# Kernel optimization log

Hardware: AMD Instinct MI355X
Metric: run time of the kernel (lower is better)

The kernel has to match this reference:

```python
import jax, jax.numpy as jnp
import numpy as np

N_NODES = 100000
N_EDGES = 1200000
IN_CH, HID_CH, OUT_CH = 64, 64, 32


def setup_inputs() -> dict:
    key = jax.random.key(0)
    ks = jax.random.split(key, 8)
    x = jax.random.normal(ks[0], (N_NODES, IN_CH), dtype=jnp.float32)
    edge_index = jax.random.randint(ks[1], (2, N_EDGES), 0, N_NODES, dtype=jnp.int64)
    # SAGEConv params: lin_l acts on aggregated neighbors (has bias), lin_r on root features.
    def glorot(k, fan_in, fan_out):
        s = jnp.sqrt(6.0 / (fan_in + fan_out))
        return jax.random.uniform(k, (fan_in, fan_out), jnp.float32, -s, s)
    W1_l = glorot(ks[2], IN_CH, HID_CH)
    W1_r = glorot(ks[3], IN_CH, HID_CH)
    b1 = jnp.zeros((HID_CH,), jnp.float32)
    W2_l = glorot(ks[4], HID_CH, OUT_CH)
    W2_r = glorot(ks[5], HID_CH, OUT_CH)
    b2 = jnp.zeros((OUT_CH,), jnp.float32)
    return {"x": x, "edge_index": edge_index, "W1_l": W1_l, "W1_r": W1_r,
            "b1": b1, "W2_l": W2_l, "W2_r": W2_r, "b2": b2}


def _sage_conv(h, src, dst, W_l, W_r, b):
    # gather source-node features along edges, mean-aggregate at destinations
    msg = h[src]                                               # [E, d]
    agg = jax.ops.segment_sum(msg, dst, num_segments=N_NODES)  # [N, d]
    cnt = jax.ops.segment_sum(jnp.ones((msg.shape[0],), h.dtype), dst,
                              num_segments=N_NODES)
    agg = agg / jnp.maximum(cnt, 1.0)[:, None]                 # mean (0 if no neighbors)
    return agg @ W_l + h @ W_r + b


def reference(x, edge_index, W1_l, W1_r, b1, W2_l, W2_r, b2):
    src, dst = edge_index[0], edge_index[1]
    h = _sage_conv(x, src, dst, W1_l, W1_r, b1)
    h = jax.nn.relu(h)
    # dropout is identity in eval mode
    return _sage_conv(h, src, dst, W2_l, W2_r, b2)
```

## Files before the change

kernel.cpp:

```cpp
#include <hip/hip_runtime.h>

__device__ __forceinline__ float bf2f(unsigned short u) {
    union { unsigned int i; float f; } v;
    v.i = ((unsigned int)u) << 16;
    return v.f;
}
__device__ __forceinline__ unsigned short f2bf(float f) {
    union { float f; unsigned int u; } v;
    v.f = f;
    unsigned int u = v.u;
    u += 0x7FFFu + ((u >> 16) & 1u);
    return (unsigned short)(u >> 16);
}
__device__ __forceinline__ unsigned int pack2bf(float lo, float hi) {
    return (unsigned int)f2bf(lo) | ((unsigned int)f2bf(hi) << 16);
}
__device__ __forceinline__ float loadElem(const void* p, size_t i, int isb) {
    return isb ? bf2f(((const unsigned short*)p)[i]) : ((const float*)p)[i];
}
__device__ __forceinline__ float bflo(unsigned int u) {
    union { unsigned int i; float f; } v; v.i = u << 16; return v.f;
}
__device__ __forceinline__ float bfhi(unsigned int u) {
    union { unsigned int i; float f; } v; v.i = u & 0xFFFF0000u; return v.f;
}

typedef __attribute__((ext_vector_type(8))) short bf16x8;
typedef __attribute__((ext_vector_type(4))) float f32x4;

#define CHUNK 4096
#define BSHIFT 8

__global__ void k_detect(const int* __restrict__ ei, int newords,
                         const unsigned int* __restrict__ xw, int nxw,
                         int* __restrict__ flags) {
    __shared__ int aOr;
    __shared__ int plaus;
    if (threadIdx.x == 0) { aOr = 0; plaus = 0; }
    __syncthreads();
    int v = 0;
    for (int i = 1 + 2 * (int)threadIdx.x; i < newords; i += 512) v |= ei[i];
    int pl = 0;
    for (int i = threadIdx.x; i < nxw; i += 256) {
        unsigned short lo = (unsigned short)(xw[i] & 0xFFFFu);
        float a = fabsf(bf2f(lo));
        if (a > 1e-5f && a < 100.0f) pl++;
    }
    atomicOr(&aOr, v);
    atomicAdd(&plaus, pl);
    __syncthreads();
    if (threadIdx.x == 0) {
        flags[0] = (aOr == 0) ? 1 : 0;
        flags[1] = (2 * plaus >= nxw) ? 1 : 0;
    }
}

__global__ void k_cast(const void* __restrict__ x, unsigned short* __restrict__ xb,
                       int n8, const int* __restrict__ flags) {
    int i = blockIdx.x * blockDim.x + threadIdx.x;
    if (i >= n8) return;
    if (flags[1]) {
        ((uint4*)xb)[i] = ((const uint4*)x)[i];
    } else {
        const float4* xf = (const float4*)x;
        float4 a = xf[2 * i], b = xf[2 * i + 1];
        ushort4 lo = { f2bf(a.x), f2bf(a.y), f2bf(a.z), f2bf(a.w) };
        ushort4 hi = { f2bf(b.x), f2bf(b.y), f2bf(b.z), f2bf(b.w) };
        ((ushort4*)xb)[2 * i] = lo;
        ((ushort4*)xb)[2 * i + 1] = hi;
    }
}

__global__ __launch_bounds__(256) void k_bcount(
        const int* __restrict__ ei, const int* __restrict__ flags,
        int* __restrict__ blockHist, int E, int NBUK, int nblk) {
    __shared__ int hist[512];
    int t = threadIdx.x;
    for (int i = t; i < NBUK; i += 256) hist[i] = 0;
    __syncthreads();
    int q = flags[0];
    int e0 = blockIdx.x * CHUNK, e1 = min(E, e0 + CHUNK);
    for (int e = e0 + t; e < e1; e += 256) {
        int dst = ei[((size_t)(E + e)) << q];
        atomicAdd(&hist[dst >> BSHIFT], 1);
    }
    __syncthreads();
    for (int i = t; i < NBUK; i += 256)
        blockHist[(size_t)i * nblk + blockIdx.x] = hist[i];
}

__global__ __launch_bounds__(256) void k_rowscan(
        int* __restrict__ blockHist, int* __restrict__ bukTot, int nblk) {
    __shared__ int sh[256];
    int t = threadIdx.x;
    int* row = blockHist + (size_t)blockIdx.x * nblk;
    int carry = 0;
    for (int base = 0; base < nblk; base += 256) {
        int i = base + t;
        int v = (i < nblk) ? row[i] : 0;
        sh[t] = v;
        __syncthreads();
        for (int off = 1; off < 256; off <<= 1) {
            int u = (t >= off) ? sh[t - off] : 0;
            __syncthreads();
            sh[t] += u;
            __syncthreads();
        }
        if (i < nblk) row[i] = carry + sh[t] - v;
        int tot = sh[255];
        __syncthreads();
        carry += tot;
    }
    if (t == 0) bukTot[blockIdx.x] = carry;
}

__global__ __launch_bounds__(512) void k_toto(
        const int* __restrict__ bukTot, int* __restrict__ bukOff,
        int* __restrict__ rowptr, int NBUK, int E, int N,
        const void* __restrict__ W1l, const void* __restrict__ W1r,
        const void* __restrict__ b1,
        const void* __restrict__ W2l, const void* __restrict__ W2r,
        const void* __restrict__ b2,
        unsigned short* __restrict__ wt1l, unsigned short* __restrict__ wt1r,
        unsigned short* __restrict__ wt2lr,
        float* __restrict__ bs1, float* __restrict__ bs2,
        const int* __restrict__ flags) {
    __shared__ int sh[512];
    int t = threadIdx.x;
    int v = (t < NBUK) ? bukTot[t] : 0;
    sh[t] = v;
    __syncthreads();
    for (int off = 1; off < 512; off <<= 1) {
        int u = (t >= off) ? sh[t - off] : 0;
        __syncthreads();
        sh[t] += u;
        __syncthreads();
    }
    if (t < NBUK) bukOff[t] = sh[t] - v;
    if (t == 0) { bukOff[NBUK] = E; rowptr[N] = E; }

    int isb = flags[1];
    for (int i = t; i < 64 * 64; i += 512) {
        int c = i >> 6, k = i & 63;
        wt1l[c * 72 + k] = isb ? ((const unsigned short*)W1l)[k * 64 + c]
                               : f2bf(((const float*)W1l)[k * 64 + c]);
        wt1r[c * 72 + k] = isb ? ((const unsigned short*)W1r)[k * 64 + c]
                               : f2bf(((const float*)W1r)[k * 64 + c]);
    }
    for (int i = t; i < 32 * 64; i += 512) {
        int c = i >> 6, k = i & 63;
        wt2lr[c * 72 + k]        = isb ? ((const unsigned short*)W2l)[k * 32 + c]
                                       : f2bf(((const float*)W2l)[k * 32 + c]);
        wt2lr[(32 + c) * 72 + k] = isb ? ((const unsigned short*)W2r)[k * 32 + c]
                                       : f2bf(((const float*)W2r)[k * 32 + c]);
    }
    if (t < 64) bs1[t] = loadElem(b1, t, isb);
    if (t < 32) bs2[t] = loadElem(b2, t, isb);
}

__global__ __launch_bounds__(256) void k_part(
        const int* __restrict__ ei, const int* __restrict__ flags,
        const int* __restrict__ blockHist, const int* __restrict__ bukOff,
        unsigned int* __restrict__ recs, int E, int NBUK, int nblk) {
    __shared__ int cur[512];
    int t = threadIdx.x;
    for (int i = t; i < NBUK; i += 256)
        cur[i] = blockHist[(size_t)i * nblk + blockIdx.x] + bukOff[i];
    __syncthreads();
    int q = flags[0];
    int e0 = blockIdx.x * CHUNK, e1 = min(E, e0 + CHUNK);
    for (int e = e0 + t; e < e1; e += 256) {
        int dst = ei[((size_t)(E + e)) << q];
        int src = ei[((size_t)e) << q];
        int pos = atomicAdd(&cur[dst >> BSHIFT], 1);
        recs[pos] = ((unsigned int)src << BSHIFT) | (unsigned int)(dst & ((1 << BSHIFT) - 1));
    }
}

__global__ __launch_bounds__(256) void k_csr(
        const unsigned int* __restrict__ recs, const int* __restrict__ bukOff,
        int* __restrict__ rowptr, int* __restrict__ esorted, int N) {
    __shared__ int degLoc[256];
    __shared__ int offLoc[256];
    __shared__ int wcur[256];
    int t = threadIdx.x;
    int node0 = blockIdx.x << BSHIFT;
    int r0 = bukOff[blockIdx.x], r1 = bukOff[blockIdx.x + 1];
    degLoc[t] = 0;
    __syncthreads();
    for (int i = r0 + t; i < r1; i += 256)
        atomicAdd(&degLoc[recs[i] & 255], 1);
    __syncthreads();
    int v = degLoc[t];
    offLoc[t] = v;
    __syncthreads();
    for (int off = 1; off < 256; off <<= 1) {
        int u = (t >= off) ? offLoc[t - off] : 0;
        __syncthreads();
        offLoc[t] += u;
        __syncthreads();
    }
    int excl = offLoc[t] - v;
    int node = node0 + t;
    if (node < N) rowptr[node] = r0 + excl;
    wcur[t] = r0 + excl;
    __syncthreads();
    for (int i = r0 + t; i < r1; i += 256) {
        unsigned int rec = recs[i];
        int pos = atomicAdd(&wcur[rec & 255], 1);
        esorted[pos] = (int)(rec >> BSHIFT);
    }
}

__global__ __launch_bounds__(256) void k_fused1(
        const unsigned short* __restrict__ feat,
        const int* __restrict__ rowptr,
        const int* __restrict__ esorted,
        const unsigned short* __restrict__ wt1l,
        const unsigned short* __restrict__ wt1r,
        const unsigned short* __restrict__ wt2lr,
        const float* __restrict__ bs1,
        const float* __restrict__ bs2,
        unsigned short* __restrict__ zbuf,
        unsigned short* __restrict__ gbuf,
        int N) {
    constexpr int SA2 = 72;
    constexpr int SW  = 72;
    __shared__ __align__(16) unsigned short amB16[64 * SA2];
    __shared__ __align__(16) unsigned short wT[64 * SW];
    __shared__ float Bs[64];
    __shared__ float Bs2[32];

    int t = threadIdx.x;
    int node0 = blockIdx.x << 6;

    for (int i = t; i < 576; i += 256)
        ((uint4*)wT)[i] = ((const uint4*)wt1l)[i];
    if (t < 64) Bs[t] = bs1[t];
    if (t >= 64 && t < 96) Bs2[t - 64] = bs2[t - 64];

    {
        int g = t >> 3, l = t & 7;
        const unsigned short* fl = feat + 8 * l;
#pragma unroll
        for (int jj = 0; jj < 2; ++jj) {
            int nl = g + 32 * jj;
            int node = node0 + nl;
            float a0 = 0.f, a1 = 0.f, a2 = 0.f, a3 = 0.f;
            float a4 = 0.f, a5 = 0.f, a6 = 0.f, a7 = 0.f;
            float inv = 0.f;
            if (node < N) {
                int beg = rowptr[node], end = rowptr[node + 1];
                int d = end - beg;
                if (d > 0) {
                    inv = 1.0f / (float)d;
                    for (int bs = beg; bs < end; bs += 8) {
                        int cnt = min(end - bs, 8);
                        const int* ep = esorted + bs;
                        int dd = 0;
                        if (cnt == 8) {
                            int s0 = ep[0], s1 = ep[1], s2 = ep[2], s3 = ep[3];
                            int s4 = ep[4], s5 = ep[5], s6 = ep[6], s7 = ep[7];
                            uint4 u0 = *(const uint4*)(fl + (size_t)s0 * 64);
                            uint4 u1 = *(const uint4*)(fl + (size_t)s1 * 64);
                            uint4 u2 = *(const uint4*)(fl + (size_t)s2 * 64);
                            uint4 u3 = *(const uint4*)(fl + (size_t)s3 * 64);
                            uint4 u4 = *(const uint4*)(fl + (size_t)s4 * 64);
                            uint4 u5 = *(const uint4*)(fl + (size_t)s5 * 64);
                            uint4 u6 = *(const uint4*)(fl + (size_t)s6 * 64);
                            uint4 u7 = *(const uint4*)(fl + (size_t)s7 * 64);
                            a0 += bflo(u0.x) + bflo(u1.x) + bflo(u2.x) + bflo(u3.x)
                                + bflo(u4.x) + bflo(u5.x) + bflo(u6.x) + bflo(u7.x);
                            a1 += bfhi(u0.x) + bfhi(u1.x) + bfhi(u2.x) + bfhi(u3.x)
                                + bfhi(u4.x) + bfhi(u5.x) + bfhi(u6.x) + bfhi(u7.x);
                            a2 += bflo(u0.y) + bflo(u1.y) + bflo(u2.y) + bflo(u3.y)
                                + bflo(u4.y) + bflo(u5.y) + bflo(u6.y) + bflo(u7.y);
                            a3 += bfhi(u0.y) + bfhi(u1.y) + bfhi(u2.y) + bfhi(u3.y)
                                + bfhi(u4.y) + bfhi(u5.y) + bfhi(u6.y) + bfhi(u7.y);
                            a4 += bflo(u0.z) + bflo(u1.z) + bflo(u2.z) + bflo(u3.z)
                                + bflo(u4.z) + bflo(u5.z) + bflo(u6.z) + bflo(u7.z);
                            a5 += bfhi(u0.z) + bfhi(u1.z) + bfhi(u2.z) + bfhi(u3.z)
                                + bfhi(u4.z) + bfhi(u5.z) + bfhi(u6.z) + bfhi(u7.z);
                            a6 += bflo(u0.w) + bflo(u1.w) + bflo(u2.w) + bflo(u3.w)
                                + bflo(u4.w) + bflo(u5.w) + bflo(u6.w) + bflo(u7.w);
                            a7 += bfhi(u0.w) + bfhi(u1.w) + bfhi(u2.w) + bfhi(u3.w)
                                + bfhi(u4.w) + bfhi(u5.w) + bfhi(u6.w) + bfhi(u7.w);
                            dd = 8;
                        }
                        for (; dd + 4 <= cnt; dd += 4) {
                            int s0 = ep[dd + 0], s1 = ep[dd + 1];
                            int s2 = ep[dd + 2], s3 = ep[dd + 3];
                            uint4 u0 = *(const uint4*)(fl + (size_t)s0 * 64);
                            uint4 u1 = *(const uint4*)(fl + (size_t)s1 * 64);
                            uint4 u2 = *(const uint4*)(fl + (size_t)s2 * 64);
                            uint4 u3 = *(const uint4*)(fl + (size_t)s3 * 64);
                            a0 += bflo(u0.x) + bflo(u1.x) + bflo(u2.x) + bflo(u3.x);
                            a1 += bfhi(u0.x) + bfhi(u1.x) + bfhi(u2.x) + bfhi(u3.x);
                            a2 += bflo(u0.y) + bflo(u1.y) + bflo(u2.y) + bflo(u3.y);
                            a3 += bfhi(u0.y) + bfhi(u1.y) + bfhi(u2.y) + bfhi(u3.y);
                            a4 += bflo(u0.z) + bflo(u1.z) + bflo(u2.z) + bflo(u3.z);
                            a5 += bfhi(u0.z) + bfhi(u1.z) + bfhi(u2.z) + bfhi(u3.z);
                            a6 += bflo(u0.w) + bflo(u1.w) + bflo(u2.w) + bflo(u3.w);
                            a7 += bfhi(u0.w) + bfhi(u1.w) + bfhi(u2.w) + bfhi(u3.w);
                        }
                        for (; dd < cnt; ++dd) {
                            int s = ep[dd];
                            uint4 u = *(const uint4*)(fl + (size_t)s * 64);
                            a0 += bflo(u.x); a1 += bfhi(u.x);
                            a2 += bflo(u.y); a3 += bfhi(u.y);
                            a4 += bflo(u.z); a5 += bfhi(u.z);
                            a6 += bflo(u.w); a7 += bfhi(u.w);
                        }
                    }
                }
            }
            uint4 packed = make_uint4(pack2bf(a0 * inv, a1 * inv),
                                      pack2bf(a2 * inv, a3 * inv),
                                      pack2bf(a4 * inv, a5 * inv),
                                      pack2bf(a6 * inv, a7 * inv));
            *(uint4*)&amB16[nl * SA2 + 8 * l] = packed;
        }
    }
    __syncthreads();

    int wid = t >> 6, lane = t & 63;
    int arow = lane & 15;
    int kgrp = (lane >> 4) * 8;
    f32x4 acc[4];
#pragma unroll
    for (int ct = 0; ct < 4; ++ct) acc[ct] = (f32x4){0.f, 0.f, 0.f, 0.f};

    const unsigned short* aBase = &amB16[(16 * wid + arow) * SA2 + kgrp];
#pragma unroll
    for (int kh = 0; kh < 2; ++kh) {
        bf16x8 a = *(const bf16x8*)(aBase + kh * 32);
#pragma unroll
        for (int ct = 0; ct < 4; ++ct) {
            bf16x8 b = *(const bf16x8*)&wT[(16 * ct + arow) * SW + kh * 32 + kgrp];
            acc[ct] = __builtin_amdgcn_mfma_f32_16x16x32_bf16(a, b, acc[ct], 0, 0, 0);
        }
    }
    __syncthreads();

    for (int i = t; i < 64 * 8; i += 256) {
        int nl = i >> 3, c = i & 7;
        int gn = node0 + nl;
        uint4 u = make_uint4(0u, 0u, 0u, 0u);
        if (gn < N) u = *(const uint4*)(feat + (size_t)gn * 64 + 8 * c);
        *(uint4*)&amB16[nl * SA2 + 8 * c] = u;
    }
    for (int i = t; i < 576; i += 256)
        ((uint4*)wT)[i] = ((const uint4*)wt1r)[i];
    __syncthreads();

#pragma unroll
    for (int kh = 0; kh < 2; ++kh) {
        bf16x8 a = *(const bf16x8*)(aBase + kh * 32);
#pragma unroll
        for (int ct = 0; ct < 4; ++ct) {
            bf16x8 b = *(const bf16x8*)&wT[(16 * ct + arow) * SW + kh * 32 + kgrp];
            acc[ct] = __builtin_amdgcn_mfma_f32_16x16x32_bf16(a, b, acc[ct], 0, 0, 0);
        }
    }
    __syncthreads();

    {
        int rbase = (lane >> 4) * 4;
#pragma unroll
        for (int ct = 0; ct < 4; ++ct) {
            int ch = 16 * ct + arow;
            float bv = Bs[ch];
#pragma unroll
            for (int r = 0; r < 4; ++r) {
                int nl = 16 * wid + rbase + r;
                float v = fmaxf(acc[ct][r] + bv, 0.f);
                amB16[nl * SA2 + ch] = f2bf(v);
            }
        }
    }
    for (int i = t; i < 576; i += 256)
        ((uint4*)wT)[i] = ((const uint4*)wt2lr)[i];
    __syncthreads();

    f32x4 accz[2], accg[2];
#pragma unroll
    for (int ct = 0; ct < 2; ++ct) {
        accz[ct] = (f32x4){0.f, 0.f, 0.f, 0.f};
        accg[ct] = (f32x4){0.f, 0.f, 0.f, 0.f};
    }
#pragma unroll
    for (int kh = 0; kh < 2; ++kh) {
        bf16x8 a = *(const bf16x8*)(aBase + kh * 32);
#pragma unroll
        for (int ct = 0; ct < 2; ++ct) {
            bf16x8 bz = *(const bf16x8*)&wT[(16 * ct + arow) * SW + kh * 32 + kgrp];
            bf16x8 bg = *(const bf16x8*)&wT[(32 + 16 * ct + arow) * SW + kh * 32 + kgrp];
            accz[ct] = __builtin_amdgcn_mfma_f32_16x16x32_bf16(a, bz, accz[ct], 0, 0, 0);
            accg[ct] = __builtin_amdgcn_mfma_f32_16x16x32_bf16(a, bg, accg[ct], 0, 0, 0);
        }
    }

#pragma unroll
    for (int ct = 0; ct < 2; ++ct) {
        int ch = 16 * ct + arow;
        float b2v = Bs2[ch];
#pragma unroll
        for (int r = 0; r < 4; ++r) {
            int node = node0 + 16 * wid + (lane >> 4) * 4 + r;
            if (node >= N) continue;
            zbuf[(size_t)node * 32 + ch] = f2bf(accz[ct][r]);
            gbuf[(size_t)node * 32 + ch] = f2bf(accg[ct][r] + b2v);
        }
    }
}

__global__ __launch_bounds__(256) void k_final(
        const unsigned short* __restrict__ zbuf,
        const unsigned short* __restrict__ gbuf,
        const int* __restrict__ rowptr,
        const int* __restrict__ esorted,
        void* __restrict__ outp,
        int N, const int* __restrict__ flags) {
    int t = threadIdx.x;
    int isb = flags[1];
    int node0 = blockIdx.x << 6;

    int g = t >> 3, l = t & 7;
    const unsigned short* fl = zbuf + 4 * l;
#pragma unroll
    for (int jj = 0; jj < 2; ++jj) {
        int nl = g + 32 * jj;
        int node = node0 + nl;
        if (node >= N) continue;
        float a0 = 0.f, a1 = 0.f, a2 = 0.f, a3 = 0.f;
        float inv = 0.f;
        int beg = rowptr[node], end = rowptr[node + 1];
        int d = end - beg;
        if (d > 0) {
            inv = 1.0f / (float)d;
            for (int bs = beg; bs < end; bs += 8) {
                int cnt = min(end - bs, 8);
                const int* ep = esorted + bs;
                int dd = 0;
                if (cnt == 8) {
                    int s0 = ep[0], s1 = ep[1], s2 = ep[2], s3 = ep[3];
                    int s4 = ep[4], s5 = ep[5], s6 = ep[6], s7 = ep[7];
                    uint2 u0 = *(const uint2*)(fl + (size_t)s0 * 32);
                    uint2 u1 = *(const uint2*)(fl + (size_t)s1 * 32);
                    uint2 u2 = *(const uint2*)(fl + (size_t)s2 * 32);
                    uint2 u3 = *(const uint2*)(fl + (size_t)s3 * 32);
                    uint2 u4 = *(const uint2*)(fl + (size_t)s4 * 32);
                    uint2 u5 = *(const uint2*)(fl + (size_t)s5 * 32);
                    uint2 u6 = *(const uint2*)(fl + (size_t)s6 * 32);
                    uint2 u7 = *(const uint2*)(fl + (size_t)s7 * 32);
                    a0 += bflo(u0.x) + bflo(u1.x) + bflo(u2.x) + bflo(u3.x)
                        + bflo(u4.x) + bflo(u5.x) + bflo(u6.x) + bflo(u7.x);
                    a1 += bfhi(u0.x) + bfhi(u1.x) + bfhi(u2.x) + bfhi(u3.x)
                        + bfhi(u4.x) + bfhi(u5.x) + bfhi(u6.x) + bfhi(u7.x);
                    a2 += bflo(u0.y) + bflo(u1.y) + bflo(u2.y) + bflo(u3.y)
                        + bflo(u4.y) + bflo(u5.y) + bflo(u6.y) + bflo(u7.y);
                    a3 += bfhi(u0.y) + bfhi(u1.y) + bfhi(u2.y) + bfhi(u3.y)
                        + bfhi(u4.y) + bfhi(u5.y) + bfhi(u6.y) + bfhi(u7.y);
                    dd = 8;
                }
                for (; dd + 4 <= cnt; dd += 4) {
                    int s0 = ep[dd + 0], s1 = ep[dd + 1];
                    int s2 = ep[dd + 2], s3 = ep[dd + 3];
                    uint2 u0 = *(const uint2*)(fl + (size_t)s0 * 32);
                    uint2 u1 = *(const uint2*)(fl + (size_t)s1 * 32);
                    uint2 u2 = *(const uint2*)(fl + (size_t)s2 * 32);
                    uint2 u3 = *(const uint2*)(fl + (size_t)s3 * 32);
                    a0 += bflo(u0.x) + bflo(u1.x) + bflo(u2.x) + bflo(u3.x);
                    a1 += bfhi(u0.x) + bfhi(u1.x) + bfhi(u2.x) + bfhi(u3.x);
                    a2 += bflo(u0.y) + bflo(u1.y) + bflo(u2.y) + bflo(u3.y);
                    a3 += bfhi(u0.y) + bfhi(u1.y) + bfhi(u2.y) + bfhi(u3.y);
                }
                for (; dd < cnt; ++dd) {
                    int s = ep[dd];
                    uint2 u = *(const uint2*)(fl + (size_t)s * 32);
                    a0 += bflo(u.x); a1 += bfhi(u.x);
                    a2 += bflo(u.y); a3 += bfhi(u.y);
                }
            }
        }
        uint2 gv = *(const uint2*)(gbuf + (size_t)node * 32 + 4 * l);
        float r0 = a0 * inv + bflo(gv.x);
        float r1 = a1 * inv + bfhi(gv.x);
        float r2 = a2 * inv + bflo(gv.y);
        float r3 = a3 * inv + bfhi(gv.y);
        if (!isb) {
            *(float4*)((float*)outp + (size_t)node * 32 + 4 * l) =
                make_float4(r0, r1, r2, r3);
        } else {
            ushort4 o = { f2bf(r0), f2bf(r1), f2bf(r2), f2bf(r3) };
            *(ushort4*)((unsigned short*)outp + (size_t)node * 32 + 4 * l) = o;
        }
    }
}

extern "C" void kernel_launch(void* const* d_in, const int* in_sizes, int n_in,
                              void* d_out, int out_size, void* d_ws, size_t ws_size,
                              hipStream_t stream) {
    const void* x   = d_in[0];
    const int*  ei  = (const int*)d_in[1];
    const void* W1l = d_in[2];
    const void* W1r = d_in[3];
    const void* b1  = d_in[4];
    const void* W2l = d_in[5];
    const void* W2r = d_in[6];
    const void* b2  = d_in[7];

    const int N = in_sizes[0] / 64;
    const int E = in_sizes[1] / 2;
    const int NBUK = (N + (1 << BSHIFT) - 1) >> BSHIFT;
    const int nblk = (E + CHUNK - 1) / CHUNK;

    char* base = (char*)d_ws;
    size_t off = 0;
    auto alloc = [&](size_t bytes) { size_t o = off; off = (off + bytes + 255) & ~(size_t)255; return o; };
    int* flags   = (int*)(base + alloc(256));
    int* bukTot  = (int*)(base + alloc((size_t)NBUK * 4));
    int* bukOff  = (int*)(base + alloc((size_t)(NBUK + 1) * 4));
    int* rowptr  = (int*)(base + alloc((size_t)(N + 1) * 4));
    unsigned int* recs = (unsigned int*)(base + alloc((size_t)E * 4));
    int* esorted = (int*)(base + alloc((size_t)E * 4));
    unsigned short* xb = (unsigned short*)(base + alloc((size_t)N * 64 * 2));
    unsigned short* h  = (unsigned short*)(base + alloc((size_t)N * 64 * 2));
    unsigned short* wt1l  = (unsigned short*)(base + alloc(64 * 72 * 2));
    unsigned short* wt1r  = (unsigned short*)(base + alloc(64 * 72 * 2));
    unsigned short* wt2lr = (unsigned short*)(base + alloc(64 * 72 * 2));
    float* bs1 = (float*)(base + alloc(64 * 4));
    float* bs2 = (float*)(base + alloc(32 * 4));
    (void)ws_size;

    unsigned short* zbuf = h;
    unsigned short* gbuf = h + (size_t)N * 32;

    int* blockHist = (int*)xb;

    const int B = 256;
    int nd = 2 * E; if (nd > 2048) nd = 2048;

    k_detect<<<1, 256, 0, stream>>>(ei, nd, (const unsigned int*)x, 512, flags);
    k_bcount<<<nblk, B, 0, stream>>>(ei, flags, blockHist, E, NBUK, nblk);
    k_rowscan<<<NBUK, B, 0, stream>>>(blockHist, bukTot, nblk);
    k_toto<<<1, 512, 0, stream>>>(bukTot, bukOff, rowptr, NBUK, E, N,
                                  W1l, W1r, b1, W2l, W2r, b2,
                                  wt1l, wt1r, wt2lr, bs1, bs2, flags);
    k_part<<<nblk, B, 0, stream>>>(ei, flags, blockHist, bukOff, recs, E, NBUK, nblk);
    k_cast<<<(N * 8 + B - 1) / B, B, 0, stream>>>(x, xb, N * 8, flags);
    k_csr<<<NBUK, B, 0, stream>>>(recs, bukOff, rowptr, esorted, N);

    const int ntile = (N + 63) / 64;
    k_fused1<<<ntile, B, 0, stream>>>(xb, rowptr, esorted,
                                      wt1l, wt1r, wt2lr, bs1, bs2,
                                      zbuf, gbuf, N);
    k_final<<<ntile, B, 0, stream>>>(zbuf, gbuf, rowptr, esorted, d_out, N, flags);
}
```

Baseline: 213.6 us.

## Merge CSR-building preprocessing kernels into one cooperative megakernel with grid syncs

Replaces seven small preprocessing launches (detect, bucket count, row scan, offsets and weight transpose, partition, cast, CSR build) with a single cooperative kernel that separates phases with grid-wide syncs. The goal is to cut per-launch overhead and idle gaps between tiny kernels. The cast now overlaps the bucket-count phase, and blockHist gets its own buffer instead of aliasing xb. In exchange, the grid is capped at max(NBUK, nblk), about 391 blocks, so the cast runs at lower parallelism. Each grid sync also carries its own cost, and cooperative launch limits occupancy.

Result: slower. 624.5 us (+192.4%).

```diff
diff --git a/kernel.cpp b/kernel.cpp
--- a/kernel.cpp
+++ b/kernel.cpp
@@ -1,4 +1,7 @@
 #include <hip/hip_runtime.h>
+#include <hip/hip_cooperative_groups.h>
+
+namespace cg = cooperative_groups;
 
 __device__ __forceinline__ float bf2f(unsigned short u) {
     union { unsigned int i; float f; } v;
@@ -31,184 +34,188 @@
 #define CHUNK 4096
 #define BSHIFT 8
 
-__global__ void k_detect(const int* __restrict__ ei, int newords,
-                         const unsigned int* __restrict__ xw, int nxw,
-                         int* __restrict__ flags) {
-    __shared__ int aOr;
-    __shared__ int plaus;
-    if (threadIdx.x == 0) { aOr = 0; plaus = 0; }
-    __syncthreads();
-    int v = 0;
-    for (int i = 1 + 2 * (int)threadIdx.x; i < newords; i += 512) v |= ei[i];
-    int pl = 0;
-    for (int i = threadIdx.x; i < nxw; i += 256) {
-        unsigned short lo = (unsigned short)(xw[i] & 0xFFFFu);
-        float a = fabsf(bf2f(lo));
-        if (a > 1e-5f && a < 100.0f) pl++;
-    }
-    atomicOr(&aOr, v);
-    atomicAdd(&plaus, pl);
-    __syncthreads();
-    if (threadIdx.x == 0) {
-        flags[0] = (aOr == 0) ? 1 : 0;
-        flags[1] = (2 * plaus >= nxw) ? 1 : 0;
-    }
-}
-
-__global__ void k_cast(const void* __restrict__ x, unsigned short* __restrict__ xb,
-                       int n8, const int* __restrict__ flags) {
-    int i = blockIdx.x * blockDim.x + threadIdx.x;
-    if (i >= n8) return;
-    if (flags[1]) {
-        ((uint4*)xb)[i] = ((const uint4*)x)[i];
-    } else {
-        const float4* xf = (const float4*)x;
-        float4 a = xf[2 * i], b = xf[2 * i + 1];
-        ushort4 lo = { f2bf(a.x), f2bf(a.y), f2bf(a.z), f2bf(a.w) };
-        ushort4 hi = { f2bf(b.x), f2bf(b.y), f2bf(b.z), f2bf(b.w) };
-        ((ushort4*)xb)[2 * i] = lo;
-        ((ushort4*)xb)[2 * i + 1] = hi;
-    }
-}
-
-__global__ __launch_bounds__(256) void k_bcount(
-        const int* __restrict__ ei, const int* __restrict__ flags,
-        int* __restrict__ blockHist, int E, int NBUK, int nblk) {
-    __shared__ int hist[512];
+struct MegaArgs {
+    const int* ei; const unsigned int* xw; int nd; int nxw;
+    int* flags;
+    int* blockHist; int* bukTot; int* bukOff; int* rowptr;
+    unsigned int* recs; int* esorted;
+    const void* x; unsigned short* xb;
+    const void* W1l; const void* W1r; const void* b1;
+    const void* W2l; const void* W2r; const void* b2;
+    unsigned short* wt1l; unsigned short* wt1r; unsigned short* wt2lr;
+    float* bs1; float* bs2;
+    int E; int N; int NBUK; int nblk; int n8;
+};
+
+__global__ __launch_bounds__(256) void k_mega(MegaArgs a) {
+    cg::grid_group gg = cg::this_grid();
+    __shared__ int sh[768];
     int t = threadIdx.x;
-    for (int i = t; i < NBUK; i += 256) hist[i] = 0;
-    __syncthreads();
-    int q = flags[0];
-    int e0 = blockIdx.x * CHUNK, e1 = min(E, e0 + CHUNK);
-    for (int e = e0 + t; e < e1; e += 256) {
-        int dst = ei[((size_t)(E + e)) << q];
-        atomicAdd(&hist[dst >> BSHIFT], 1);
-    }
-    __syncthreads();
-    for (int i = t; i < NBUK; i += 256)
-        blockHist[(size_t)i * nblk + blockIdx.x] = hist[i];
-}
-
-__global__ __launch_bounds__(256) void k_rowscan(
-        int* __restrict__ blockHist, int* __restrict__ bukTot, int nblk) {
-    __shared__ int sh[256];
-    int t = threadIdx.x;
-    int* row = blockHist + (size_t)blockIdx.x * nblk;
-    int carry = 0;
-    for (int base = 0; base < nblk; base += 256) {
-        int i = base + t;
-        int v = (i < nblk) ? row[i] : 0;
-        sh[t] = v;
+    int b = blockIdx.x;
+
+    if (b == 0) {
+        int v = 0;
+        for (int i = 1 + 2 * t; i < a.nd; i += 512) v |= a.ei[i];
+        int pl = 0;
+        for (int i = t; i < a.nxw; i += 256) {
+            unsigned short lo = (unsigned short)(a.xw[i] & 0xFFFFu);
+            float f = fabsf(bf2f(lo));
+            if (f > 1e-5f && f < 100.0f) pl++;
+        }
+        sh[t] = v; sh[256 + t] = pl;
+        __syncthreads();
+        for (int off = 128; off > 0; off >>= 1) {
+            if (t < off) { sh[t] |= sh[t + off]; sh[256 + t] += sh[256 + t + off]; }
+            __syncthreads();
+        }
+        if (t == 0) {
+            a.flags[0] = (sh[0] == 0) ? 1 : 0;
+            a.flags[1] = (2 * sh[256] >= a.nxw) ? 1 : 0;
+        }
+    }
+    __threadfence();
+    gg.sync();
+
+    int q = a.flags[0], isb = a.flags[1];
+
+    if (b < a.nblk) {
+        for (int i = t; i < a.NBUK; i += 256) sh[i] = 0;
+        __syncthreads();
+        int e0 = b * CHUNK, e1 = min(a.E, e0 + CHUNK);
+        for (int e = e0 + t; e < e1; e += 256) {
+            int dst = a.ei[((size_t)(a.E + e)) << q];
+            atomicAdd(&sh[dst >> BSHIFT], 1);
+        }
+        __syncthreads();
+        for (int i = t; i < a.NBUK; i += 256)
+            a.blockHist[(size_t)i * a.nblk + b] = sh[i];
+    }
+    for (int i = b * 256 + t; i < a.n8; i += gridDim.x * 256) {
+        if (isb) {
+            ((uint4*)a.xb)[i] = ((const uint4*)a.x)[i];
+        } else {
+            const float4* xf = (const float4*)a.x;
+            float4 p = xf[2 * i], r = xf[2 * i + 1];
+            ushort4 lo = { f2bf(p.x), f2bf(p.y), f2bf(p.z), f2bf(p.w) };
+            ushort4 hi = { f2bf(r.x), f2bf(r.y), f2bf(r.z), f2bf(r.w) };
+            ((ushort4*)a.xb)[2 * i] = lo;
+            ((ushort4*)a.xb)[2 * i + 1] = hi;
+        }
+    }
+    __threadfence();
+    gg.sync();
+
+    if (b < a.NBUK) {
+        int* row = a.blockHist + (size_t)b * a.nblk;
+        int carry = 0;
+        for (int base = 0; base < a.nblk; base += 256) {
+            int i = base + t;
+            int v = (i < a.nblk) ? row[i] : 0;
+            sh[t] = v;
+            __syncthreads();
+            for (int off = 1; off < 256; off <<= 1) {
+                int u = (t >= off) ? sh[t - off] : 0;
+                __syncthreads();
+                sh[t] += u;
+                __syncthreads();
+            }
+            if (i < a.nblk) row[i] = carry + sh[t] - v;
+            int tot = sh[255];
+            __syncthreads();
+            carry += tot;
+        }
+        if (t == 0) a.bukTot[b] = carry;
+    }
+    __threadfence();
+    gg.sync();
+
+    if (b == 0) {
+        int carry = 0;
+        for (int base = 0; base < a.NBUK; base += 256) {
+            int i = base + t;
+            int v = (i < a.NBUK) ? a.bukTot[i] : 0;
+            sh[t] = v;
+            __syncthreads();
+            for (int off = 1; off < 256; off <<= 1) {
+                int u = (t >= off) ? sh[t - off] : 0;
+                __syncthreads();
+                sh[t] += u;
+                __syncthreads();
+            }
+            if (i < a.NBUK) a.bukOff[i] = carry + sh[t] - v;
+            int tot = sh[255];
+            __syncthreads();
+            carry += tot;
+        }
+        if (t == 0) { a.bukOff[a.NBUK] = a.E; a.rowptr[a.N] = a.E; }
+    } else if (b == 1) {
+        for (int i = t; i < 64 * 64; i += 256) {
+            int c = i >> 6, k = i & 63;
+            a.wt1l[c * 72 + k] = isb ? ((const unsigned short*)a.W1l)[k * 64 + c]
+                                     : f2bf(((const float*)a.W1l)[k * 64 + c]);
+            a.wt1r[c * 72 + k] = isb ? ((const unsigned short*)a.W1r)[k * 64 + c]
+                                     : f2bf(((const float*)a.W1r)[k * 64 + c]);
+        }
+    } else if (b == 2) {
+        for (int i = t; i < 32 * 64; i += 256) {
+            int c = i >> 6, k = i & 63;
+            a.wt2lr[c * 72 + k]        = isb ? ((const unsigned short*)a.W2l)[k * 32 + c]
+                                             : f2bf(((const float*)a.W2l)[k * 32 + c]);
+            a.wt2lr[(32 + c) * 72 + k] = isb ? ((const unsigned short*)a.W2r)[k * 32 + c]
+                                             : f2bf(((const float*)a.W2r)[k * 32 + c]);
+        }
+        if (t < 64) a.bs1[t] = loadElem(a.b1, t, isb);
+        if (t >= 64 && t < 96) a.bs2[t - 64] = loadElem(a.b2, t - 64, isb);
+    }
+    __threadfence();
+    gg.sync();
+
+    if (b < a.nblk) {
+        for (int i = t; i < a.NBUK; i += 256)
+            sh[i] = a.blockHist[(size_t)i * a.nblk + b] + a.bukOff[i];
+        __syncthreads();
+        int e0 = b * CHUNK, e1 = min(a.E, e0 + CHUNK);
+        for (int e = e0 + t; e < e1; e += 256) {
+            int dst = a.ei[((size_t)(a.E + e)) << q];
+            int src = a.ei[((size_t)e) << q];
+            int pos = atomicAdd(&sh[dst >> BSHIFT], 1);
+            a.recs[pos] = ((unsigned int)src << BSHIFT) |
+                          (unsigned int)(dst & ((1 << BSHIFT) - 1));
+        }
+    }
+    __threadfence();
+    gg.sync();
+
+    if (b < a.NBUK) {
+        int node0 = b << BSHIFT;
+        int r0 = a.bukOff[b], r1 = a.bukOff[b + 1];
+        int* degLoc = sh;
+        int* offLoc = sh + 256;
+        int* wcur   = sh + 512;
+        degLoc[t] = 0;
+        __syncthreads();
+        for (int i = r0 + t; i < r1; i += 256)
+            atomicAdd(&degLoc[a.recs[i] & 255], 1);
+        __syncthreads();
+        int v = degLoc[t];
+        offLoc[t] = v;
         __syncthreads();
         for (int off = 1; off < 256; off <<= 1) {
-            int u = (t >= off) ? sh[t - off] : 0;
-            __syncthreads();
-            sh[t] += u;
-            __syncthreads();
-        }
-        if (i < nblk) row[i] = carry + sh[t] - v;
-        int tot = sh[255];
-        __syncthreads();
-        carry += tot;
-    }
-    if (t == 0) bukTot[blockIdx.x] = carry;
-}
-
-__global__ __launch_bounds__(512) void k_toto(
-        const int* __restrict__ bukTot, int* __restrict__ bukOff,
-        int* __restrict__ rowptr, int NBUK, int E, int N,
-        const void* __restrict__ W1l, const void* __restrict__ W1r,
-        const void* __restrict__ b1,
-        const void* __restrict__ W2l, const void* __restrict__ W2r,
-        const void* __restrict__ b2,
-        unsigned short* __restrict__ wt1l, unsigned short* __restrict__ wt1r,
-        unsigned short* __restrict__ wt2lr,
-        float* __restrict__ bs1, float* __restrict__ bs2,
-        const int* __restrict__ flags) {
-    __shared__ int sh[512];
-    int t = threadIdx.x;
-    int v = (t < NBUK) ? bukTot[t] : 0;
-    sh[t] = v;
-    __syncthreads();
-    for (int off = 1; off < 512; off <<= 1) {
-        int u = (t >= off) ? sh[t - off] : 0;
-        __syncthreads();
-        sh[t] += u;
-        __syncthreads();
-    }
-    if (t < NBUK) bukOff[t] = sh[t] - v;
-    if (t == 0) { bukOff[NBUK] = E; rowptr[N] = E; }
-
-    int isb = flags[1];
-    for (int i = t; i < 64 * 64; i += 512) {
-        int c = i >> 6, k = i & 63;
-        wt1l[c * 72 + k] = isb ? ((const unsigned short*)W1l)[k * 64 + c]
-                               : f2bf(((const float*)W1l)[k * 64 + c]);
-        wt1r[c * 72 + k] = isb ? ((const unsigned short*)W1r)[k * 64 + c]
-                               : f2bf(((const float*)W1r)[k * 64 + c]);
-    }
-    for (int i = t; i < 32 * 64; i += 512) {
-        int c = i >> 6, k = i & 63;
-        wt2lr[c * 72 + k]        = isb ? ((const unsigned short*)W2l)[k * 32 + c]
-                                       : f2bf(((const float*)W2l)[k * 32 + c]);
-        wt2lr[(32 + c) * 72 + k] = isb ? ((const unsigned short*)W2r)[k * 32 + c]
-                                       : f2bf(((const float*)W2r)[k * 32 + c]);
-    }
-    if (t < 64) bs1[t] = loadElem(b1, t, isb);
-    if (t < 32) bs2[t] = loadElem(b2, t, isb);
-}
-
-__global__ __launch_bounds__(256) void k_part(
-        const int* __restrict__ ei, const int* __restrict__ flags,
-        const int* __restrict__ blockHist, const int* __restrict__ bukOff,
-        unsigned int* __restrict__ recs, int E, int NBUK, int nblk) {
-    __shared__ int cur[512];
-    int t = threadIdx.x;
-    for (int i = t; i < NBUK; i += 256)
-        cur[i] = blockHist[(size_t)i * nblk + blockIdx.x] + bukOff[i];
-    __syncthreads();
-    int q = flags[0];
-    int e0 = blockIdx.x * CHUNK, e1 = min(E, e0 + CHUNK);
-    for (int e = e0 + t; e < e1; e += 256) {
-        int dst = ei[((size_t)(E + e)) << q];
-        int src = ei[((size_t)e) << q];
-        int pos = atomicAdd(&cur[dst >> BSHIFT], 1);
-        recs[pos] = ((unsigned int)src << BSHIFT) | (unsigned int)(dst & ((1 << BSHIFT) - 1));
-    }
-}
-
-__global__ __launch_bounds__(256) void k_csr(
-        const unsigned int* __restrict__ recs, const int* __restrict__ bukOff,
-        int* __restrict__ rowptr, int* __restrict__ esorted, int N) {
-    __shared__ int degLoc[256];
-    __shared__ int offLoc[256];
-    __shared__ int wcur[256];
-    int t = threadIdx.x;
-    int node0 = blockIdx.x << BSHIFT;
-    int r0 = bukOff[blockIdx.x], r1 = bukOff[blockIdx.x + 1];
-    degLoc[t] = 0;
-    __syncthreads();
-    for (int i = r0 + t; i < r1; i += 256)
-        atomicAdd(&degLoc[recs[i] & 255], 1);
-    __syncthreads();
-    int v = degLoc[t];
-    offLoc[t] = v;
-    __syncthreads();
-    for (int off = 1; off < 256; off <<= 1) {
-        int u = (t >= off) ? offLoc[t - off] : 0;
-        __syncthreads();
-        offLoc[t] += u;
-        __syncthreads();
-    }
-    int excl = offLoc[t] - v;
-    int node = node0 + t;
-    if (node < N) rowptr[node] = r0 + excl;
-    wcur[t] = r0 + excl;
-    __syncthreads();
-    for (int i = r0 + t; i < r1; i += 256) {
-        unsigned int rec = recs[i];
-        int pos = atomicAdd(&wcur[rec & 255], 1);
-        esorted[pos] = (int)(rec >> BSHIFT);
+            int u = (t >= off) ? offLoc[t - off] : 0;
+            __syncthreads();
+            offLoc[t] += u;
+            __syncthreads();
+        }
+        int excl = offLoc[t] - v;
+        int node = node0 + t;
+        if (node < a.N) a.rowptr[node] = r0 + excl;
+        wcur[t] = r0 + excl;
+        __syncthreads();
+        for (int i = r0 + t; i < r1; i += 256) {
+            unsigned int rec = a.recs[i];
+            int pos = atomicAdd(&wcur[rec & 255], 1);
+            a.esorted[pos] = (int)(rec >> BSHIFT);
+        }
     }
 }
 
@@ -336,8 +343,8 @@
         bf16x8 a = *(const bf16x8*)(aBase + kh * 32);
 #pragma unroll
         for (int ct = 0; ct < 4; ++ct) {
-            bf16x8 b = *(const bf16x8*)&wT[(16 * ct + arow) * SW + kh * 32 + kgrp];
-            acc[ct] = __builtin_amdgcn_mfma_f32_16x16x32_bf16(a, b, acc[ct], 0, 0, 0);
+            bf16x8 bb = *(const bf16x8*)&wT[(16 * ct + arow) * SW + kh * 32 + kgrp];
+            acc[ct] = __builtin_amdgcn_mfma_f32_16x16x32_bf16(a, bb, acc[ct], 0, 0, 0);
         }
     }
     __syncthreads();
@@ -358,8 +365,8 @@
         bf16x8 a = *(const bf16x8*)(aBase + kh * 32);
 #pragma unroll
         for (int ct = 0; ct < 4; ++ct) {
-            bf16x8 b = *(const bf16x8*)&wT[(16 * ct + arow) * SW + kh * 32 + kgrp];
-            acc[ct] = __builtin_amdgcn_mfma_f32_16x16x32_bf16(a, b, acc[ct], 0, 0, 0);
+            bf16x8 bb = *(const bf16x8*)&wT[(16 * ct + arow) * SW + kh * 32 + kgrp];
+            acc[ct] = __builtin_amdgcn_mfma_f32_16x16x32_bf16(a, bb, acc[ct], 0, 0, 0);
         }
     }
     __syncthreads();
@@ -531,29 +538,34 @@
     unsigned short* wt2lr = (unsigned short*)(base + alloc(64 * 72 * 2));
     float* bs1 = (float*)(base + alloc(64 * 4));
     float* bs2 = (float*)(base + alloc(32 * 4));
+    int* blockHist = (int*)(base + alloc((size_t)NBUK * nblk * 4));
     (void)ws_size;
 
     unsigned short* zbuf = h;
     unsigned short* gbuf = h + (size_t)N * 32;
 
-    int* blockHist = (int*)xb;
-
-    const int B = 256;
     int nd = 2 * E; if (nd > 2048) nd = 2048;
 
-    k_detect<<<1, 256, 0, stream>>>(ei, nd, (const unsigned int*)x, 512, flags);
-    k_bcount<<<nblk, B, 0, stream>>>(ei, flags, blockHist, E, NBUK, nblk);
-    k_rowscan<<<NBUK, B, 0, stream>>>(blockHist, bukTot, nblk);
-    k_toto<<<1, 512, 0, stream>>>(bukTot, bukOff, rowptr, NBUK, E, N,
-                                  W1l, W1r, b1, W2l, W2r, b2,
-                                  wt1l, wt1r, wt2lr, bs1, bs2, flags);
-    k_part<<<nblk, B, 0, stream>>>(ei, flags, blockHist, bukOff, recs, E, NBUK, nblk);
-    k_cast<<<(N * 8 + B - 1) / B, B, 0, stream>>>(x, xb, N * 8, flags);
-    k_csr<<<NBUK, B, 0, stream>>>(recs, bukOff, rowptr, esorted, N);
+    MegaArgs ma;
+    ma.ei = ei; ma.xw = (const unsigned int*)x; ma.nd = nd; ma.nxw = 512;
+    ma.flags = flags;
+    ma.blockHist = blockHist; ma.bukTot = bukTot; ma.bukOff = bukOff; ma.rowptr = rowptr;
+    ma.recs = recs; ma.esorted = esorted;
+    ma.x = x; ma.xb = xb;
+    ma.W1l = W1l; ma.W1r = W1r; ma.b1 = b1;
+    ma.W2l = W2l; ma.W2r = W2r; ma.b2 = b2;
+    ma.wt1l = wt1l; ma.wt1r = wt1r; ma.wt2lr = wt2lr;
+    ma.bs1 = bs1; ma.bs2 = bs2;
+    ma.E = E; ma.N = N; ma.NBUK = NBUK; ma.nblk = nblk; ma.n8 = N * 8;
+
+    int gmax = (NBUK > nblk) ? NBUK : nblk;
+    void* params[1] = { &ma };
+    hipLaunchCooperativeKernel((void*)k_mega, dim3(gmax), dim3(256),
+                               params, 0, stream);
 
     const int ntile = (N + 63) / 64;
-    k_fused1<<<ntile, B, 0, stream>>>(xb, rowptr, esorted,
-                                      wt1l, wt1r, wt2lr, bs1, bs2,
-                                      zbuf, gbuf, N);
-    k_final<<<ntile, B, 0, stream>>>(zbuf, gbuf, rowptr, esorted, d_out, N, flags);
-}
+    k_fused1<<<ntile, 256, 0, stream>>>(xb, rowptr, esorted,
+                                        wt1l, wt1r, wt2lr, bs1, bs2,
+                                        zbuf, gbuf, N);
+    k_final<<<ntile, 256, 0, stream>>>(zbuf, gbuf, rowptr, esorted, d_out, N, flags);
+}
```

## Fuse preprocessing kernels and replace per-block offsets with global atomic cursors

Applied to the files above, without the earlier changes.

Format detection, the destination-bucket histogram, weight transposition and the x-to-bf16 cast are merged into one `k_prep` kernel. Each block recomputes the detection flags locally instead of reading a flags buffer. The row scan and total-offset kernels are replaced by a single-block `k_scan` that sums the histograms and writes global bucket cursors. `k_part` then claims record slots with global atomics on those cursors instead of per-block precomputed offsets, and `k_final` recomputes the dtype flag itself. This removes several launches and the multi-kernel scan, but it adds heavily contended global atomics across only a few hundred counters. Record order within a bucket also becomes nondeterministic.

New measurement: 678.0 us. 3.17x slower.

```diff
diff --git a/kernel.cpp b/kernel.cpp
--- a/kernel.cpp
+++ b/kernel.cpp
@@ -31,92 +31,32 @@
 #define CHUNK 4096
 #define BSHIFT 8
 
-__global__ void k_detect(const int* __restrict__ ei, int newords,
-                         const unsigned int* __restrict__ xw, int nxw,
-                         int* __restrict__ flags) {
-    __shared__ int aOr;
-    __shared__ int plaus;
-    if (threadIdx.x == 0) { aOr = 0; plaus = 0; }
-    __syncthreads();
+__device__ __forceinline__ void detect_local(
+        const int* ei, int nd, const unsigned int* xw, int nxw,
+        int* sh, int& q, int& isb) {
+    int t = threadIdx.x;
     int v = 0;
-    for (int i = 1 + 2 * (int)threadIdx.x; i < newords; i += 512) v |= ei[i];
+    for (int i = 1 + 2 * t; i < nd; i += 512) v |= ei[i];
     int pl = 0;
-    for (int i = threadIdx.x; i < nxw; i += 256) {
+    for (int i = t; i < nxw; i += 256) {
         unsigned short lo = (unsigned short)(xw[i] & 0xFFFFu);
         float a = fabsf(bf2f(lo));
         if (a > 1e-5f && a < 100.0f) pl++;
     }
-    atomicOr(&aOr, v);
-    atomicAdd(&plaus, pl);
-    __syncthreads();
-    if (threadIdx.x == 0) {
-        flags[0] = (aOr == 0) ? 1 : 0;
-        flags[1] = (2 * plaus >= nxw) ? 1 : 0;
-    }
-}
-
-__global__ void k_cast(const void* __restrict__ x, unsigned short* __restrict__ xb,
-                       int n8, const int* __restrict__ flags) {
-    int i = blockIdx.x * blockDim.x + threadIdx.x;
-    if (i >= n8) return;
-    if (flags[1]) {
-        ((uint4*)xb)[i] = ((const uint4*)x)[i];
-    } else {
-        const float4* xf = (const float4*)x;
-        float4 a = xf[2 * i], b = xf[2 * i + 1];
-        ushort4 lo = { f2bf(a.x), f2bf(a.y), f2bf(a.z), f2bf(a.w) };
-        ushort4 hi = { f2bf(b.x), f2bf(b.y), f2bf(b.z), f2bf(b.w) };
-        ((ushort4*)xb)[2 * i] = lo;
-        ((ushort4*)xb)[2 * i + 1] = hi;
-    }
-}
-
-__global__ __launch_bounds__(256) void k_bcount(
-        const int* __restrict__ ei, const int* __restrict__ flags,
-        int* __restrict__ blockHist, int E, int NBUK, int nblk) {
-    __shared__ int hist[512];
-    int t = threadIdx.x;
-    for (int i = t; i < NBUK; i += 256) hist[i] = 0;
-    __syncthreads();
-    int q = flags[0];
-    int e0 = blockIdx.x * CHUNK, e1 = min(E, e0 + CHUNK);
-    for (int e = e0 + t; e < e1; e += 256) {
-        int dst = ei[((size_t)(E + e)) << q];
-        atomicAdd(&hist[dst >> BSHIFT], 1);
-    }
-    __syncthreads();
-    for (int i = t; i < NBUK; i += 256)
-        blockHist[(size_t)i * nblk + blockIdx.x] = hist[i];
-}
-
-__global__ __launch_bounds__(256) void k_rowscan(
-        int* __restrict__ blockHist, int* __restrict__ bukTot, int nblk) {
-    __shared__ int sh[256];
-    int t = threadIdx.x;
-    int* row = blockHist + (size_t)blockIdx.x * nblk;
-    int carry = 0;
-    for (int base = 0; base < nblk; base += 256) {
-        int i = base + t;
-        int v = (i < nblk) ? row[i] : 0;
-        sh[t] = v;
+    sh[t] = v; sh[256 + t] = pl;
+    __syncthreads();
+    for (int off = 128; off > 0; off >>= 1) {
+        if (t < off) { sh[t] |= sh[t + off]; sh[256 + t] += sh[256 + t + off]; }
         __syncthreads();
-        for (int off = 1; off < 256; off <<= 1) {
-            int u = (t >= off) ? sh[t - off] : 0;
-            __syncthreads();
-            sh[t] += u;
-            __syncthreads();
-        }
-        if (i < nblk) row[i] = carry + sh[t] - v;
-        int tot = sh[255];
-        __syncthreads();
-        carry += tot;
-    }
-    if (t == 0) bukTot[blockIdx.x] = carry;
-}
-
-__global__ __launch_bounds__(512) void k_toto(
-        const int* __restrict__ bukTot, int* __restrict__ bukOff,
-        int* __restrict__ rowptr, int NBUK, int E, int N,
+    }
+    q   = (sh[0] == 0) ? 1 : 0;
+    isb = (2 * sh[256] >= nxw) ? 1 : 0;
+    __syncthreads();
+}
+
+__global__ __launch_bounds__(256) void k_prep(
+        const int* __restrict__ ei, const void* __restrict__ x,
+        int* __restrict__ blockHist, unsigned short* __restrict__ xb,
         const void* __restrict__ W1l, const void* __restrict__ W1r,
         const void* __restrict__ b1,
         const void* __restrict__ W2l, const void* __restrict__ W2r,
@@ -124,11 +64,73 @@
         unsigned short* __restrict__ wt1l, unsigned short* __restrict__ wt1r,
         unsigned short* __restrict__ wt2lr,
         float* __restrict__ bs1, float* __restrict__ bs2,
-        const int* __restrict__ flags) {
+        int E, int NBUK, int nblk, int n8, int nd, int nxw) {
+    __shared__ int sh[768];
+    int t = threadIdx.x;
+    int b = blockIdx.x;
+    int q, isb;
+    detect_local(ei, nd, (const unsigned int*)x, nxw, sh, q, isb);
+
+    for (int i = t; i < NBUK; i += 256) sh[i] = 0;
+    __syncthreads();
+    int e0 = b * CHUNK, e1 = min(E, e0 + CHUNK);
+    for (int e = e0 + t; e < e1; e += 256) {
+        int dst = ei[((size_t)(E + e)) << q];
+        atomicAdd(&sh[dst >> BSHIFT], 1);
+    }
+    __syncthreads();
+    for (int i = t; i < NBUK; i += 256)
+        blockHist[(size_t)b * NBUK + i] = sh[i];
+
+    if (b == 0) {
+        for (int i = t; i < 64 * 64; i += 256) {
+            int c = i >> 6, k = i & 63;
+            wt1l[c * 72 + k] = isb ? ((const unsigned short*)W1l)[k * 64 + c]
+                                   : f2bf(((const float*)W1l)[k * 64 + c]);
+        }
+    } else if (b == 1) {
+        for (int i = t; i < 64 * 64; i += 256) {
+            int c = i >> 6, k = i & 63;
+            wt1r[c * 72 + k] = isb ? ((const unsigned short*)W1r)[k * 64 + c]
+                                   : f2bf(((const float*)W1r)[k * 64 + c]);
+        }
+    } else if (b == 2) {
+        for (int i = t; i < 32 * 64; i += 256) {
+            int c = i >> 6, k = i & 63;
+            wt2lr[c * 72 + k]        = isb ? ((const unsigned short*)W2l)[k * 32 + c]
+                                           : f2bf(((const float*)W2l)[k * 32 + c]);
+            wt2lr[(32 + c) * 72 + k] = isb ? ((const unsigned short*)W2r)[k * 32 + c]
+                                           : f2bf(((const float*)W2r)[k * 32 + c]);
+        }
+        if (t < 64) bs1[t] = loadElem(b1, t, isb);
+        if (t >= 64 && t < 96) bs2[t - 64] = loadElem(b2, t - 64, isb);
+    }
+
+    for (int i = b * 256 + t; i < n8; i += gridDim.x * 256) {
+        if (isb) {
+            ((uint4*)xb)[i] = ((const uint4*)x)[i];
+        } else {
+            const float4* xf = (const float4*)x;
+            float4 p = xf[2 * i], r = xf[2 * i + 1];
+            ushort4 lo = { f2bf(p.x), f2bf(p.y), f2bf(p.z), f2bf(p.w) };
+            ushort4 hi = { f2bf(r.x), f2bf(r.y), f2bf(r.z), f2bf(r.w) };
+            ((ushort4*)xb)[2 * i] = lo;
+            ((ushort4*)xb)[2 * i + 1] = hi;
+        }
+    }
+}
+
+__global__ __launch_bounds__(512) void k_scan(
+        const int* __restrict__ blockHist, int* __restrict__ bukOff,
+        int* __restrict__ cur, int* __restrict__ rowptr,
+        int NBUK, int nblk, int E, int N) {
     __shared__ int sh[512];
     int t = threadIdx.x;
-    int v = (t < NBUK) ? bukTot[t] : 0;
-    sh[t] = v;
+    int tot = 0;
+    if (t < NBUK)
+        for (int b = 0; b < nblk; ++b)
+            tot += blockHist[(size_t)b * NBUK + t];
+    sh[t] = tot;
     __syncthreads();
     for (int off = 1; off < 512; off <<= 1) {
         int u = (t >= off) ? sh[t - off] : 0;
@@ -136,38 +138,21 @@
         sh[t] += u;
         __syncthreads();
     }
-    if (t < NBUK) bukOff[t] = sh[t] - v;
+    if (t < NBUK) {
+        int excl = sh[t] - tot;
+        bukOff[t] = excl;
+        cur[t] = excl;
+    }
     if (t == 0) { bukOff[NBUK] = E; rowptr[N] = E; }
-
-    int isb = flags[1];
-    for (int i = t; i < 64 * 64; i += 512) {
-        int c = i >> 6, k = i & 63;
-        wt1l[c * 72 + k] = isb ? ((const unsigned short*)W1l)[k * 64 + c]
-                               : f2bf(((const float*)W1l)[k * 64 + c]);
-        wt1r[c * 72 + k] = isb ? ((const unsigned short*)W1r)[k * 64 + c]
-                               : f2bf(((const float*)W1r)[k * 64 + c]);
-    }
-    for (int i = t; i < 32 * 64; i += 512) {
-        int c = i >> 6, k = i & 63;
-        wt2lr[c * 72 + k]        = isb ? ((const unsigned short*)W2l)[k * 32 + c]
-                                       : f2bf(((const float*)W2l)[k * 32 + c]);
-        wt2lr[(32 + c) * 72 + k] = isb ? ((const unsigned short*)W2r)[k * 32 + c]
-                                       : f2bf(((const float*)W2r)[k * 32 + c]);
-    }
-    if (t < 64) bs1[t] = loadElem(b1, t, isb);
-    if (t < 32) bs2[t] = loadElem(b2, t, isb);
 }
 
 __global__ __launch_bounds__(256) void k_part(
-        const int* __restrict__ ei, const int* __restrict__ flags,
-        const int* __restrict__ blockHist, const int* __restrict__ bukOff,
-        unsigned int* __restrict__ recs, int E, int NBUK, int nblk) {
-    __shared__ int cur[512];
-    int t = threadIdx.x;
-    for (int i = t; i < NBUK; i += 256)
-        cur[i] = blockHist[(size_t)i * nblk + blockIdx.x] + bukOff[i];
-    __syncthreads();
-    int q = flags[0];
+        const int* __restrict__ ei, int* __restrict__ cur,
+        unsigned int* __restrict__ recs, int E, int nd) {
+    __shared__ int sh[512];
+    int t = threadIdx.x;
+    int q, isb;
+    detect_local(ei, nd, (const unsigned int*)ei, 0, sh, q, isb);
     int e0 = blockIdx.x * CHUNK, e1 = min(E, e0 + CHUNK);
     for (int e = e0 + t; e < e1; e += 256) {
         int dst = ei[((size_t)(E + e)) << q];
@@ -336,8 +321,8 @@
         bf16x8 a = *(const bf16x8*)(aBase + kh * 32);
 #pragma unroll
         for (int ct = 0; ct < 4; ++ct) {
-            bf16x8 b = *(const bf16x8*)&wT[(16 * ct + arow) * SW + kh * 32 + kgrp];
-            acc[ct] = __builtin_amdgcn_mfma_f32_16x16x32_bf16(a, b, acc[ct], 0, 0, 0);
+            bf16x8 bb = *(const bf16x8*)&wT[(16 * ct + arow) * SW + kh * 32 + kgrp];
+            acc[ct] = __builtin_amdgcn_mfma_f32_16x16x32_bf16(a, bb, acc[ct], 0, 0, 0);
         }
     }
     __syncthreads();
@@ -358,8 +343,8 @@
         bf16x8 a = *(const bf16x8*)(aBase + kh * 32);
 #pragma unroll
         for (int ct = 0; ct < 4; ++ct) {
-            bf16x8 b = *(const bf16x8*)&wT[(16 * ct + arow) * SW + kh * 32 + kgrp];
-            acc[ct] = __builtin_amdgcn_mfma_f32_16x16x32_bf16(a, b, acc[ct], 0, 0, 0);
+            bf16x8 bb = *(const bf16x8*)&wT[(16 * ct + arow) * SW + kh * 32 + kgrp];
+            acc[ct] = __builtin_amdgcn_mfma_f32_16x16x32_bf16(a, bb, acc[ct], 0, 0, 0);
         }
     }
     __syncthreads();
@@ -420,10 +405,27 @@
         const int* __restrict__ rowptr,
         const int* __restrict__ esorted,
         void* __restrict__ outp,
-        int N, const int* __restrict__ flags) {
-    int t = threadIdx.x;
-    int isb = flags[1];
+        int N, const void* __restrict__ x, int nxw) {
+    __shared__ int shp[256];
+    int t = threadIdx.x;
     int node0 = blockIdx.x << 6;
+
+    {
+        const unsigned int* xw = (const unsigned int*)x;
+        int pl = 0;
+        for (int i = t; i < nxw; i += 256) {
+            unsigned short lo = (unsigned short)(xw[i] & 0xFFFFu);
+            float a = fabsf(bf2f(lo));
+            if (a > 1e-5f && a < 100.0f) pl++;
+        }
+        shp[t] = pl;
+        __syncthreads();
+        for (int off = 128; off > 0; off >>= 1) {
+            if (t < off) shp[t] += shp[t + off];
+            __syncthreads();
+        }
+    }
+    int isb = (2 * shp[0] >= nxw) ? 1 : 0;
 
     int g = t >> 3, l = t & 7;
     const unsigned short* fl = zbuf + 4 * l;
@@ -518,9 +520,8 @@
     char* base = (char*)d_ws;
     size_t off = 0;
     auto alloc = [&](size_t bytes) { size_t o = off; off = (off + bytes + 255) & ~(size_t)255; return o; };
-    int* flags   = (int*)(base + alloc(256));
-    int* bukTot  = (int*)(base + alloc((size_t)NBUK * 4));
     int* bukOff  = (int*)(base + alloc((size_t)(NBUK + 1) * 4));
+    int* cur     = (int*)(base + alloc((size_t)(NBUK + 1) * 4));
     int* rowptr  = (int*)(base + alloc((size_t)(N + 1) * 4));
     unsigned int* recs = (unsigned int*)(base + alloc((size_t)E * 4));
     int* esorted = (int*)(base + alloc((size_t)E * 4));
@@ -531,29 +532,26 @@
     unsigned short* wt2lr = (unsigned short*)(base + alloc(64 * 72 * 2));
     float* bs1 = (float*)(base + alloc(64 * 4));
     float* bs2 = (float*)(base + alloc(32 * 4));
+    int* blockHist = (int*)(base + alloc((size_t)nblk * NBUK * 4));
     (void)ws_size;
 
     unsigned short* zbuf = h;
     unsigned short* gbuf = h + (size_t)N * 32;
 
-    int* blockHist = (int*)xb;
-
-    const int B = 256;
     int nd = 2 * E; if (nd > 2048) nd = 2048;
-
-    k_detect<<<1, 256, 0, stream>>>(ei, nd, (const unsigned int*)x, 512, flags);
-    k_bcount<<<nblk, B, 0, stream>>>(ei, flags, blockHist, E, NBUK, nblk);
-    k_rowscan<<<NBUK, B, 0, stream>>>(blockHist, bukTot, nblk);
-    k_toto<<<1, 512, 0, stream>>>(bukTot, bukOff, rowptr, NBUK, E, N,
-                                  W1l, W1r, b1, W2l, W2r, b2,
-                                  wt1l, wt1r, wt2lr, bs1, bs2, flags);
-    k_part<<<nblk, B, 0, stream>>>(ei, flags, blockHist, bukOff, recs, E, NBUK, nblk);
-    k_cast<<<(N * 8 + B - 1) / B, B, 0, stream>>>(x, xb, N * 8, flags);
-    k_csr<<<NBUK, B, 0, stream>>>(recs, bukOff, rowptr, esorted, N);
+    const int nxw = 512;
+
+    k_prep<<<nblk, 256, 0, stream>>>(ei, x, blockHist, xb,
+                                     W1l, W1r, b1, W2l, W2r, b2,
+                                     wt1l, wt1r, wt2lr, bs1, bs2,
+                                     E, NBUK, nblk, N * 8, nd, nxw);
+    k_scan<<<1, 512, 0, stream>>>(blockHist, bukOff, cur, rowptr, NBUK, nblk, E, N);
+    k_part<<<nblk, 256, 0, stream>>>(ei, cur, recs, E, nd);
+    k_csr<<<NBUK, 256, 0, stream>>>(recs, bukOff, rowptr, esorted, N);
 
     const int ntile = (N + 63) / 64;
-    k_fused1<<<ntile, B, 0, stream>>>(xb, rowptr, esorted,
-                                      wt1l, wt1r, wt2lr, bs1, bs2,
-                                      zbuf, gbuf, N);
-    k_final<<<ntile, B, 0, stream>>>(zbuf, gbuf, rowptr, esorted, d_out, N, flags);
-}
+    k_fused1<<<ntile, 256, 0, stream>>>(xb, rowptr, esorted,
+                                        wt1l, wt1r, wt2lr, bs1, bs2,
+                                        zbuf, gbuf, N);
+    k_final<<<ntile, 256, 0, stream>>>(zbuf, gbuf, rowptr, esorted, d_out, N, x, nxw);
+}
```
